# Performance work log

Hardware: AMD Instinct MI355X
Metric: run time of the kernel (lower is better)

## Reference

```python
import math
import jax, jax.numpy as jnp
import numpy as np

ALPHA = 0.7

def setup_inputs() -> dict:
    key = jax.random.key(0)
    ks = jax.random.split(key, 4)
    T, V, Q, F, D = 256, 256, 32, 64, 512
    return {
        "text_embed": jax.random.normal(ks[0], (T, D), dtype=jnp.float32),
        "clip_embed": jax.random.normal(ks[1], (V, D), dtype=jnp.float32),
        "concept_embeds": jax.random.normal(ks[2], (T, Q, D), dtype=jnp.float32),
        "frame_embeds": jax.random.normal(ks[3], (V, F, D), dtype=jnp.float32),
        "logit_scale": jnp.array(math.log(1.0 / 0.07), dtype=jnp.float32),
    }

def _l2norm(x, eps=1e-12):
    # matches F.normalize(dim=-1): x / max(||x||, eps)
    n = jnp.sqrt(jnp.sum(x * x, axis=-1, keepdims=True))
    return x / jnp.maximum(n, eps)

def reference(text_embed, clip_embed, concept_embeds, frame_embeds, logit_scale):
    scale = jnp.minimum(jnp.exp(logit_scale), 100.0)
    # global similarity: [T, V]
    g_sim = scale * (text_embed @ clip_embed.T)
    # local MaxSim: normalize, dot products, max over frames f, mean over tokens q
    nc = _l2norm(concept_embeds.astype(jnp.float32))  # [T, Q, D]
    nf = _l2norm(frame_embeds.astype(jnp.float32))    # [V, F, D]
    scores = jnp.einsum('tqd,vfd->tvqf', nc, nf)      # [T, V, Q, F]
    max_scores = jnp.max(scores, axis=-1)             # [T, V, Q]
    l_sim = scale * jnp.mean(max_scores, axis=-1)     # [T, V]
    return ALPHA * g_sim + (1.0 - ALPHA) * l_sim
```

## Files before the change

### kernel.cpp

```cpp
#include <hip/hip_runtime.h>
#include <stdint.h>

#define ALPHA_ 0.7f
constexpr int Tn = 256, Vn = 256, Qn = 32, Fn = 64, Dn = 512;
constexpr int Mn = Tn * Qn;
constexpr int Nn = Vn * Fn;
constexpr int Kn = Dn;
constexpr int NT = Kn / 64;

typedef float  f32x4  __attribute__((ext_vector_type(4)));
typedef __bf16 bf16x8 __attribute__((ext_vector_type(8)));

static __device__ __forceinline__ unsigned short f2bf(float f) {
  uint32_t x = __builtin_bit_cast(uint32_t, f);
  x += 0x7fffu + ((x >> 16) & 1u);
  return (unsigned short)(x >> 16);
}

static __device__ __forceinline__ void gload_lds16(const void* g, void* l) {
  __builtin_amdgcn_global_load_lds(
      (const __attribute__((address_space(1))) uint32_t*)g,
      (__attribute__((address_space(3))) uint32_t*)l, 16, 0, 0);
}

#define BAR()   asm volatile("s_barrier" ::: "memory")
#define LGKM0() do { asm volatile("s_waitcnt lgkmcnt(0)" ::: "memory"); \
                     __builtin_amdgcn_sched_barrier(0); } while (0)
#define VM6()   asm volatile("s_waitcnt vmcnt(6)" ::: "memory")
#define VM0()   asm volatile("s_waitcnt vmcnt(0)" ::: "memory")

__global__ void normalize_rows(const float* __restrict__ src,
                               uint4* __restrict__ dst) {
  const int wave = threadIdx.x >> 6;
  const int lane = threadIdx.x & 63;
  const int row  = blockIdx.x * 4 + wave;
  const float4* p = reinterpret_cast<const float4*>(src + (size_t)row * Dn + lane * 8);
  float4 x0 = p[0];
  float4 x1 = p[1];
  float ss = x0.x*x0.x + x0.y*x0.y + x0.z*x0.z + x0.w*x0.w
           + x1.x*x1.x + x1.y*x1.y + x1.z*x1.z + x1.w*x1.w;
  #pragma unroll
  for (int m = 1; m < 64; m <<= 1) ss += __shfl_xor(ss, m, 64);
  const float inv = 1.0f / fmaxf(sqrtf(ss), 1e-12f);
  union { unsigned short u[8]; uint4 v; } pk;
  const float f[8] = {x0.x, x0.y, x0.z, x0.w, x1.x, x1.y, x1.z, x1.w};
  #pragma unroll
  for (int j = 0; j < 8; ++j) pk.u[j] = f2bf(f[j] * inv);
  dst[(size_t)row * (Dn / 8) + lane] = pk.v;
}

__global__ __launch_bounds__(512, 2)
void maxsim256_kernel(const uint16_t* __restrict__ Abf,
                      const uint16_t* __restrict__ Bbf,
                      const float* __restrict__ text,
                      const float* __restrict__ clip,
                      const float* __restrict__ logit_scale,
                      float* __restrict__ out) {
  __shared__ __align__(16) unsigned char lds[131072];
  const int tid  = threadIdx.x;
  const int lane = tid & 63;
  const int wave = tid >> 6;
  const int wr   = wave >> 2;
  const int wc   = wave & 3;
  const int bx   = blockIdx.x;
  const int by   = blockIdx.y;

  const char* Ag = reinterpret_cast<const char*>(Abf) + (size_t)by * 256 * 1024;
  const char* Bg = reinterpret_cast<const char*>(Bbf) + (size_t)bx * 256 * 1024;

  auto stage = [&](int buf, int isB, int h, int tile) {
    const char* g = isB ? Bg : Ag;
    const unsigned base = buf * 65536 + isB * 32768 + h * 16384;
    #pragma unroll
    for (int j = 0; j < 2; ++j) {
      const unsigned flat = (j * 8 + wave) * 1024 + lane * 16;
      const unsigned r = flat >> 7, c0 = flat & 127;
      const unsigned R = isB ? ((r >> 5) << 6) + h * 32 + (r & 31)
                             : ((r >> 6) << 7) + h * 64 + (r & 63);
      gload_lds16(g + (size_t)R * 1024 + tile * 128 + (c0 ^ ((r & 7) << 4)),
                  &lds[base + (j * 8 + wave) * 1024]);
    }
  };

  f32x4 acc[8][4];
  #pragma unroll
  for (int i = 0; i < 8; ++i)
    #pragma unroll
    for (int j = 0; j < 4; ++j)
      acc[i][j] = {0.f, 0.f, 0.f, 0.f};

  bf16x8 af[4][2];
  bf16x8 bq[4][2];

  const int rA  = lane & 15;
  const int kg  = lane >> 4;
  const unsigned key = (unsigned)(rA & 7) << 4;

  auto ldA = [&](int buf, int h) {
    const unsigned b = buf * 65536 + h * 16384;
    #pragma unroll
    for (int m = 0; m < 4; ++m) {
      const unsigned s = (unsigned)(wr * 64 + m * 16 + rA);
      #pragma unroll
      for (int kk = 0; kk < 2; ++kk) {
        const unsigned kb = kk * 64 + kg * 16;
        af[m][kk] = *reinterpret_cast<const bf16x8*>(&lds[b + s * 128 + (kb ^ key)]);
      }
    }
  };
  auto ldB = [&](int buf, int h) {
    const unsigned b = buf * 65536 + 32768 + h * 16384;
    #pragma unroll
    for (int n = 0; n < 2; ++n) {
      const unsigned s = (unsigned)(wc * 32 + n * 16 + rA);
      #pragma unroll
      for (int kk = 0; kk < 2; ++kk) {
        const unsigned kb = kk * 64 + kg * 16;
        bq[h * 2 + n][kk] = *reinterpret_cast<const bf16x8*>(&lds[b + s * 128 + (kb ^ key)]);
      }
    }
  };
  auto mfma_quad = [&](int hm, int hn) {
    __builtin_amdgcn_s_setprio(1);
    #pragma unroll
    for (int m = 0; m < 4; ++m)
      #pragma unroll
      for (int n = 0; n < 2; ++n)
        #pragma unroll
        for (int kk = 0; kk < 2; ++kk) {
          const int mi = hm * 4 + m, ni = hn * 2 + n;
          acc[mi][ni] = __builtin_amdgcn_mfma_f32_16x16x32_bf16(
              af[m][kk], bq[ni][kk], acc[mi][ni], 0, 0, 0);
        }
    __builtin_amdgcn_s_setprio(0);
  };

  stage(0, 0, 0, 0); stage(0, 1, 0, 0); stage(0, 1, 1, 0); stage(0, 0, 1, 0);
  stage(1, 0, 0, 1); stage(1, 1, 0, 1); stage(1, 1, 1, 1);
  VM6(); BAR();

  auto tile_step = [&](int t, int buf) {
    ldA(buf, 0); ldB(buf, 0);
    if (t + 1 < NT) stage(buf ^ 1, 0, 1, t + 1);
    asm volatile("s_waitcnt lgkmcnt(8)" ::: "memory");
    BAR(); LGKM0();
    mfma_quad(0, 0);
    BAR();
    ldB(buf, 1);
    if (t + 2 < NT) stage(buf, 0, 0, t + 2);
    BAR(); LGKM0();
    mfma_quad(0, 1);
    BAR();
    ldA(buf, 1);
    if (t + 2 < NT) stage(buf, 1, 0, t + 2);
    BAR(); LGKM0();
    mfma_quad(1, 1);
    BAR();
    if (t + 2 < NT) stage(buf, 1, 1, t + 2);
    BAR();
    mfma_quad(1, 0);
    if (t < NT - 2) { VM6(); } else { VM0(); }
    BAR();
  };

  for (int t = 0; t < NT; t += 2) {
    tile_step(t, 0);
    tile_step(t + 1, 1);
  }

  const float scale = fminf(expf(logit_scale[0]), 100.0f);
  const int v_out = bx * 4 + wc;
  const float4* cp = reinterpret_cast<const float4*>(clip + (size_t)v_out * Dn) + lane * 2;
  const float4 c0 = cp[0], c1 = cp[1];

  #pragma unroll
  for (int g = 0; g < 4; ++g) {
    float sum = 0.f;
    #pragma unroll
    for (int m2 = 0; m2 < 2; ++m2) {
      const int mi = g * 2 + m2;
      #pragma unroll
      for (int reg = 0; reg < 4; ++reg) {
        float rm = fmaxf(fmaxf(acc[mi][0][reg], acc[mi][1][reg]),
                         fmaxf(acc[mi][2][reg], acc[mi][3][reg]));
        rm = fmaxf(rm, __shfl_xor(rm, 1, 64));
        rm = fmaxf(rm, __shfl_xor(rm, 2, 64));
        rm = fmaxf(rm, __shfl_xor(rm, 4, 64));
        rm = fmaxf(rm, __shfl_xor(rm, 8, 64));
        sum += rm;
      }
    }
    sum += __shfl_xor(sum, 16, 64);
    sum += __shfl_xor(sum, 32, 64);

    const int t_out = by * 8 + wr * 4 + g;
    const float4* tp = reinterpret_cast<const float4*>(text + (size_t)t_out * Dn) + lane * 2;
    const float4 t0 = tp[0], t1 = tp[1];
    float gd = t0.x*c0.x + t0.y*c0.y + t0.z*c0.z + t0.w*c0.w
             + t1.x*c1.x + t1.y*c1.y + t1.z*c1.z + t1.w*c1.w;
    gd += __shfl_xor(gd, 1, 64);  gd += __shfl_xor(gd, 2, 64);
    gd += __shfl_xor(gd, 4, 64);  gd += __shfl_xor(gd, 8, 64);
    gd += __shfl_xor(gd, 16, 64); gd += __shfl_xor(gd, 32, 64);

    if (lane == 0)
      out[t_out * Vn + v_out] =
          ALPHA_ * scale * gd + (1.0f - ALPHA_) * scale * (sum * (1.0f / (float)Qn));
  }
}

extern "C" void kernel_launch(void* const* d_in, const int* in_sizes, int n_in,
                              void* d_out, int out_size, void* d_ws, size_t ws_size,
                              hipStream_t stream) {
  const float* text        = (const float*)d_in[0];
  const float* clip        = (const float*)d_in[1];
  const float* concept     = (const float*)d_in[2];
  const float* frames      = (const float*)d_in[3];
  const float* logit_scale = (const float*)d_in[4];
  float* out = (float*)d_out;

  uint16_t* Abf = (uint16_t*)d_ws;
  uint16_t* Bbf = Abf + (size_t)Mn * Kn;

  normalize_rows<<<Mn / 4, 256, 0, stream>>>(concept, (uint4*)Abf);
  normalize_rows<<<Nn / 4, 256, 0, stream>>>(frames, (uint4*)Bbf);
  dim3 grid(Nn / 256, Mn / 256);
  maxsim256_kernel<<<grid, 512, 0, stream>>>(Abf, Bbf, text, clip, logit_scale, out);
}
```

Measured before the change: 231.1 us.

## Make GEMM blocks persistent over eight output tiles with a continuous prefetch pipeline

The grid shrinks from 2048 blocks to 256 persistent blocks. Each block walks eight consecutive N tiles, and its global-to-LDS prefetch pipeline keeps running across tile boundaries. The per-tile epilogue runs inside the pipeline and resets the accumulators, which removes the per-block pipeline fill and drain and the launch tail. Staging address offsets are precomputed once per thread. The cost is less parallelism per CU (256 blocks across the device) and epilogue work placed on the critical path between tiles.

```diff
diff --git a/kernel.cpp b/kernel.cpp
--- a/kernel.cpp
+++ b/kernel.cpp
@@ -6,7 +6,8 @@
 constexpr int Mn = Tn * Qn;
 constexpr int Nn = Vn * Fn;
 constexpr int Kn = Dn;
-constexpr int NT = Kn / 64;
+constexpr int NOT = 8;
+constexpr int GT  = (Kn / 64) * NOT;
 
 typedef float  f32x4  __attribute__((ext_vector_type(4)));
 typedef __bf16 bf16x8 __attribute__((ext_vector_type(8)));
@@ -62,23 +63,36 @@
   const int wave = tid >> 6;
   const int wr   = wave >> 2;
   const int wc   = wave & 3;
-  const int bx   = blockIdx.x;
-  const int by   = blockIdx.y;
-
-  const char* Ag = reinterpret_cast<const char*>(Abf) + (size_t)by * 256 * 1024;
-  const char* Bg = reinterpret_cast<const char*>(Bbf) + (size_t)bx * 256 * 1024;
-
-  auto stage = [&](int buf, int isB, int h, int tile) {
-    const char* g = isB ? Bg : Ag;
+  const int bid  = blockIdx.x;
+  const int nx0  = (bid & 7) * 8;
+  const int by   = bid >> 3;
+
+  const float scale = fminf(expf(logit_scale[0]), 100.0f);
+  const float coefG = ALPHA_ * scale;
+  const float coefL = (1.0f - ALPHA_) * scale * (1.0f / (float)Qn);
+
+  const char* Ag  = reinterpret_cast<const char*>(Abf) + (size_t)by  * 262144;
+  const char* Bg0 = reinterpret_cast<const char*>(Bbf) + (size_t)nx0 * 262144;
+
+  unsigned srcA[2], srcB[2], ldsoff[2];
+  #pragma unroll
+  for (int j = 0; j < 2; ++j) {
+    const unsigned r = (j * 8 + wave) * 8 + (lane >> 3);
+    const unsigned c = (((lane & 7) ^ (lane >> 3)) << 4);
+    srcA[j]  = (((r >> 6) << 7) + (r & 63)) * 1024 + c;
+    srcB[j]  = (((r >> 5) << 6) + (r & 31)) * 1024 + c;
+    ldsoff[j] = (j * 8 + wave) * 1024;
+  }
+
+  auto stage = [&](int buf, int isB, int h, int g) {
     const unsigned base = buf * 65536 + isB * 32768 + h * 16384;
+    const unsigned kt = (g & 7) * 128;
     #pragma unroll
     for (int j = 0; j < 2; ++j) {
-      const unsigned flat = (j * 8 + wave) * 1024 + lane * 16;
-      const unsigned r = flat >> 7, c0 = flat & 127;
-      const unsigned R = isB ? ((r >> 5) << 6) + h * 32 + (r & 31)
-                             : ((r >> 6) << 7) + h * 64 + (r & 63);
-      gload_lds16(g + (size_t)R * 1024 + tile * 128 + (c0 ^ ((r & 7) << 4)),
-                  &lds[base + (j * 8 + wave) * 1024]);
+      const void* src = isB
+          ? (const void*)(Bg0 + (size_t)((g >> 3) * 262144 + h * 32768 + kt + srcB[j]))
+          : (const void*)(Ag  + (size_t)(h * 65536 + kt + srcA[j]));
+      gload_lds16(src, &lds[base + ldsoff[j]]);
     }
   };
 
@@ -135,76 +149,83 @@
     __builtin_amdgcn_s_setprio(0);
   };
 
+  auto epilogue = [&](int ot) {
+    const int v_out = (nx0 + ot) * 4 + wc;
+    const float4* cp = reinterpret_cast<const float4*>(clip + (size_t)v_out * Dn) + lane * 2;
+    const float4 c0 = cp[0], c1 = cp[1];
+    float4 t0[4], t1[4];
+    #pragma unroll
+    for (int gq = 0; gq < 4; ++gq) {
+      const float4* tp = reinterpret_cast<const float4*>(
+          text + (size_t)(by * 8 + wr * 4 + gq) * Dn) + lane * 2;
+      t0[gq] = tp[0]; t1[gq] = tp[1];
+    }
+    #pragma unroll
+    for (int gq = 0; gq < 4; ++gq) {
+      float sum = 0.f;
+      #pragma unroll
+      for (int m2 = 0; m2 < 2; ++m2) {
+        const int mi = gq * 2 + m2;
+        #pragma unroll
+        for (int reg = 0; reg < 4; ++reg) {
+          float rm = fmaxf(fmaxf(acc[mi][0][reg], acc[mi][1][reg]),
+                           fmaxf(acc[mi][2][reg], acc[mi][3][reg]));
+          rm = fmaxf(rm, __shfl_xor(rm, 1, 64));
+          rm = fmaxf(rm, __shfl_xor(rm, 2, 64));
+          rm = fmaxf(rm, __shfl_xor(rm, 4, 64));
+          rm = fmaxf(rm, __shfl_xor(rm, 8, 64));
+          sum += rm;
+        }
+      }
+      sum += __shfl_xor(sum, 16, 64);
+      sum += __shfl_xor(sum, 32, 64);
+      float gd = t0[gq].x*c0.x + t0[gq].y*c0.y + t0[gq].z*c0.z + t0[gq].w*c0.w
+               + t1[gq].x*c1.x + t1[gq].y*c1.y + t1[gq].z*c1.z + t1[gq].w*c1.w;
+      gd += __shfl_xor(gd, 1, 64);  gd += __shfl_xor(gd, 2, 64);
+      gd += __shfl_xor(gd, 4, 64);  gd += __shfl_xor(gd, 8, 64);
+      gd += __shfl_xor(gd, 16, 64); gd += __shfl_xor(gd, 32, 64);
+      if (lane == 0)
+        out[(by * 8 + wr * 4 + gq) * Vn + v_out] = coefG * gd + coefL * sum;
+    }
+    #pragma unroll
+    for (int i = 0; i < 8; ++i)
+      #pragma unroll
+      for (int j = 0; j < 4; ++j)
+        acc[i][j] = {0.f, 0.f, 0.f, 0.f};
+  };
+
   stage(0, 0, 0, 0); stage(0, 1, 0, 0); stage(0, 1, 1, 0); stage(0, 0, 1, 0);
   stage(1, 0, 0, 1); stage(1, 1, 0, 1); stage(1, 1, 1, 1);
   VM6(); BAR();
 
-  auto tile_step = [&](int t, int buf) {
+  auto tile_step = [&](int g, int buf) {
     ldA(buf, 0); ldB(buf, 0);
-    if (t + 1 < NT) stage(buf ^ 1, 0, 1, t + 1);
+    if (g + 1 < GT) stage(buf ^ 1, 0, 1, g + 1);
     asm volatile("s_waitcnt lgkmcnt(8)" ::: "memory");
     BAR(); LGKM0();
     mfma_quad(0, 0);
     BAR();
     ldB(buf, 1);
-    if (t + 2 < NT) stage(buf, 0, 0, t + 2);
+    if (g + 2 < GT) stage(buf, 0, 0, g + 2);
     BAR(); LGKM0();
     mfma_quad(0, 1);
     BAR();
     ldA(buf, 1);
-    if (t + 2 < NT) stage(buf, 1, 0, t + 2);
+    if (g + 2 < GT) stage(buf, 1, 0, g + 2);
     BAR(); LGKM0();
     mfma_quad(1, 1);
     BAR();
-    if (t + 2 < NT) stage(buf, 1, 1, t + 2);
+    if (g + 2 < GT) stage(buf, 1, 1, g + 2);
     BAR();
     mfma_quad(1, 0);
-    if (t < NT - 2) { VM6(); } else { VM0(); }
-    BAR();
-  };
-
-  for (int t = 0; t < NT; t += 2) {
+    if (g < GT - 2) { VM6(); } else { VM0(); }
+    if ((g & 7) == 7) epilogue(g >> 3);
+    BAR();
+  };
+
+  for (int t = 0; t < GT; t += 2) {
     tile_step(t, 0);
     tile_step(t + 1, 1);
-  }
-
-  const float scale = fminf(expf(logit_scale[0]), 100.0f);
-  const int v_out = bx * 4 + wc;
-  const float4* cp = reinterpret_cast<const float4*>(clip + (size_t)v_out * Dn) + lane * 2;
-  const float4 c0 = cp[0], c1 = cp[1];
-
-  #pragma unroll
-  for (int g = 0; g < 4; ++g) {
-    float sum = 0.f;
-    #pragma unroll
-    for (int m2 = 0; m2 < 2; ++m2) {
-      const int mi = g * 2 + m2;
-      #pragma unroll
-      for (int reg = 0; reg < 4; ++reg) {
-        float rm = fmaxf(fmaxf(acc[mi][0][reg], acc[mi][1][reg]),
-                         fmaxf(acc[mi][2][reg], acc[mi][3][reg]));
-        rm = fmaxf(rm, __shfl_xor(rm, 1, 64));
-        rm = fmaxf(rm, __shfl_xor(rm, 2, 64));
-        rm = fmaxf(rm, __shfl_xor(rm, 4, 64));
-        rm = fmaxf(rm, __shfl_xor(rm, 8, 64));
-        sum += rm;
-      }
-    }
-    sum += __shfl_xor(sum, 16, 64);
-    sum += __shfl_xor(sum, 32, 64);
-
-    const int t_out = by * 8 + wr * 4 + g;
-    const float4* tp = reinterpret_cast<const float4*>(text + (size_t)t_out * Dn) + lane * 2;
-    const float4 t0 = tp[0], t1 = tp[1];
-    float gd = t0.x*c0.x + t0.y*c0.y + t0.z*c0.z + t0.w*c0.w
-             + t1.x*c1.x + t1.y*c1.y + t1.z*c1.z + t1.w*c1.w;
-    gd += __shfl_xor(gd, 1, 64);  gd += __shfl_xor(gd, 2, 64);
-    gd += __shfl_xor(gd, 4, 64);  gd += __shfl_xor(gd, 8, 64);
-    gd += __shfl_xor(gd, 16, 64); gd += __shfl_xor(gd, 32, 64);
-
-    if (lane == 0)
-      out[t_out * Vn + v_out] =
-          ALPHA_ * scale * gd + (1.0f - ALPHA_) * scale * (sum * (1.0f / (float)Qn));
   }
 }
 
@@ -223,6 +244,5 @@
 
   normalize_rows<<<Mn / 4, 256, 0, stream>>>(concept, (uint4*)Abf);
   normalize_rows<<<Nn / 4, 256, 0, stream>>>(frames, (uint4*)Bbf);
-  dim3 grid(Nn / 256, Mn / 256);
-  maxsim256_kernel<<<grid, 512, 0, stream>>>(Abf, Bbf, text, clip, logit_scale, out);
-}
+  maxsim256_kernel<<<256, 512, 0, stream>>>(Abf, Bbf, text, clip, logit_scale, out);
+}
```

New measurement: 228.6 us. About the same (-1.1%).
